# Performance work log

Measured on AMD Instinct MI355X. Metric: run time of the kernel, lower is better.

The kernel has to match this reference:

```python
import jax, jax.numpy as jnp
import numpy as np

B, T, M, DK, DV, S = 64, 256, 64, 128, 256, 128
NSK, NQ = 200, 2000


def _glorot(k, shape):
    lim = np.sqrt(6.0 / (shape[0] + shape[1])).astype(np.float32)
    return jax.random.uniform(k, shape, jnp.float32, -lim, lim)


def setup_inputs() -> dict:
    key = jax.random.key(0)
    ks = jax.random.split(key, 16)
    tn = lambda k, shape: 0.1 * jax.random.truncated_normal(k, -2.0, 2.0, shape, jnp.float32)
    return {
        "q_data": jax.random.randint(ks[0], (B, T), 0, NSK + 1),
        "qa_data": jax.random.randint(ks[1], (B, T), 0, 2 * NSK + 1),
        "s_data": jax.random.randint(ks[2], (B, T), 0, NQ + 1),
        "key_memory": tn(ks[3], (M, DK)),
        "value_memory": tn(ks[4], (M, DV)),
        "Eq": 0.05 * jax.random.normal(ks[5], (NSK + 1, DK), jnp.float32),
        "Eqa": 0.05 * jax.random.normal(ks[6], (2 * NSK + 1, DV), jnp.float32),
        "Es": 0.05 * jax.random.normal(ks[7], (NQ + 1, DK), jnp.float32),
        "We": _glorot(ks[8], (DV, DV)), "be": jnp.zeros((DV,), jnp.float32),
        "Wa": _glorot(ks[9], (DV, DV)), "ba": jnp.zeros((DV,), jnp.float32),
        "Wsa": _glorot(ks[10], (DV, M)), "bsa": jnp.zeros((M,), jnp.float32),
        "Wqd1": _glorot(ks[11], (DK, S)), "bqd1": jnp.zeros((S,), jnp.float32),
        "Wqd": _glorot(ks[12], (S, 1)), "bqd": jnp.zeros((1,), jnp.float32),
        "Wsd1": _glorot(ks[13], (DK, S)), "bsd1": jnp.zeros((S,), jnp.float32),
        "Wsd": _glorot(ks[14], (S, 1)), "bsd": jnp.zeros((1,), jnp.float32),
    }


def reference(q_data, qa_data, s_data, key_memory, value_memory, Eq, Eqa, Es,
              We, be, Wa, ba, Wsa, bsa, Wqd1, bqd1, Wqd, bqd, Wsd1, bsd1, Wsd, bsd):
    b = q_data.shape[0]
    qe = Eq[q_data]    # [B,T,DK]
    qae = Eqa[qa_data]  # [B,T,DV]
    se = Es[s_data]    # [B,T,DK]
    # time-independent precomputation (same math, hoisted out of the loop)
    corr = jax.nn.softmax(jnp.einsum("btk,mk->btm", qe, key_memory), axis=-1)  # [B,T,M]
    erase = qae @ We + be  # [B,T,DV] (activation=None in source)
    add = qae @ Wa + ba    # [B,T,DV]
    qd = jnp.tanh(qe @ Wqd1 + bqd1) @ Wqd + bqd  # [B,T,1]
    sd = jnp.tanh(se @ Wsd1 + bsd1) @ Wsd + bsd  # [B,T,1]

    def step(Mv, x):
        cw, er, ad = x  # [B,M], [B,DV], [B,DV]
        read = jnp.einsum("bm,bmd->bd", cw, Mv)        # read BEFORE write
        sa1 = read @ Wsa + bsa                          # [B,M]
        sa = jnp.sum(cw * sa1, axis=1)                  # [B]
        scale = cw[:, :, None]                          # [B,M,1]
        Mv_new = Mv * (1.0 - er[:, None, :] * scale) + ad[:, None, :] * scale
        return Mv_new, sa

    Mv0 = jnp.broadcast_to(value_memory[None], (b,) + value_memory.shape)
    xs = (corr.transpose(1, 0, 2), erase.transpose(1, 0, 2), add.transpose(1, 0, 2))
    _, sa_t = jax.lax.scan(step, Mv0, xs)  # sa_t: [T,B]
    z = 3.0 * sa_t.T - qd[..., 0] - sd[..., 0]  # [B,T]
    return jax.nn.sigmoid(z)
```

## Files before the change

kernel.cpp:

```cpp
#include <hip/hip_runtime.h>
#include <math.h>

#define B_   64
#define T_   256
#define M_   64
#define DK_  128
#define DV_  256
#define S_   128
#define NQR  201
#define NQAR 401
#define NSR  2001

static __device__ __forceinline__ int imin(int a, int b){ return a < b ? a : b; }

static __device__ __forceinline__ float fast_tanh(float x){
  float e = __expf(2.f * x);
  return 1.f - 2.f / (e + 1.f);
}

template<int CTRL, int RM>
static __device__ __forceinline__ float dppadd(float x) {
  return x + __int_as_float(
      __builtin_amdgcn_update_dpp(0, __float_as_int(x), CTRL, RM, 0xf, true));
}
static __device__ __forceinline__ float wave_sum_lane63(float x) {
  x = dppadd<0x111, 0xf>(x);
  x = dppadd<0x112, 0xf>(x);
  x = dppadd<0x114, 0xf>(x);
  x = dppadd<0x118, 0xf>(x);
  x = dppadd<0x142, 0xa>(x);
  x = dppadd<0x143, 0xc>(x);
  return x;
}

__device__ void corr_role(int blk, const float* __restrict__ Eq,
                          const float* __restrict__ Km,
                          const float* __restrict__ Wsa,
                          const float* __restrict__ bsa,
                          float* __restrict__ corr,
                          float* __restrict__ w2_t,
                          float* __restrict__ csb_t)
{
  __shared__ float eq[4][DK_];
  __shared__ float cwb[4][M_];
  const int w = threadIdx.x >> 6, m = threadIdx.x & 63;
  const int i  = blk * 4 + w;
  const int ic = imin(i, NQR - 1);
  eq[w][m]      = Eq[ic * DK_ + m];
  eq[w][m + 64] = Eq[ic * DK_ + 64 + m];
  float acc = 0.f;
  const float4* kr = (const float4*)(Km + m * DK_);
  #pragma unroll 8
  for (int k4 = 0; k4 < DK_ / 4; ++k4) {
    float4 kv = kr[k4];
    acc = fmaf(eq[w][k4 * 4 + 0], kv.x, acc);
    acc = fmaf(eq[w][k4 * 4 + 1], kv.y, acc);
    acc = fmaf(eq[w][k4 * 4 + 2], kv.z, acc);
    acc = fmaf(eq[w][k4 * 4 + 3], kv.w, acc);
  }
  float mx = acc;
  #pragma unroll
  for (int off = 32; off; off >>= 1) mx = fmaxf(mx, __shfl_xor(mx, off, 64));
  float e = __expf(acc - mx);
  float ssum = e;
  #pragma unroll
  for (int off = 32; off; off >>= 1) ssum += __shfl_xor(ssum, off, 64);
  const float cw = e / ssum;
  if (i < NQR) corr[i * M_ + m] = cw;
  cwb[w][m] = cw;

  float pv = wave_sum_lane63(cw * bsa[m]);
  if (m == 63 && i < NQR) csb_t[i] = pv;

  float aw[4] = {0,0,0,0};
  for (int mm = 0; mm < M_; ++mm) {
    const float c = cwb[w][mm];
    #pragma unroll
    for (int r = 0; r < 4; ++r)
      aw[r] = fmaf(c, Wsa[(r * 64 + m) * M_ + mm], aw[r]);
  }
  if (i < NQR) {
    #pragma unroll
    for (int r = 0; r < 4; ++r) w2_t[i * DV_ + r * 64 + m] = aw[r];
  }
}

__device__ void ea_role(int blk, const float* __restrict__ Eqa,
                        const float* __restrict__ We, const float* __restrict__ be,
                        const float* __restrict__ Wa, const float* __restrict__ ba,
                        float* __restrict__ ert, float* __restrict__ adt)
{
  __shared__ float a[8][DV_];
  const int d  = threadIdx.x;
  const int i0 = blk * 8;
  #pragma unroll
  for (int r = 0; r < 8; ++r) a[r][d] = Eqa[imin(i0 + r, NQAR - 1) * DV_ + d];
  __syncthreads();
  float er[8] = {0,0,0,0,0,0,0,0}, ad[8] = {0,0,0,0,0,0,0,0};
  for (int k = 0; k < DV_; ++k) {
    float we = We[k * DV_ + d];
    float wa = Wa[k * DV_ + d];
    #pragma unroll
    for (int r = 0; r < 8; ++r) {
      er[r] = fmaf(a[r][k], we, er[r]);
      ad[r] = fmaf(a[r][k], wa, ad[r]);
    }
  }
  const float beo = be[d], bao = ba[d];
  #pragma unroll
  for (int r = 0; r < 8; ++r) {
    int i = i0 + r;
    if (i < NQAR) { ert[i * DV_ + d] = er[r] + beo; adt[i * DV_ + d] = ad[r] + bao; }
  }
}

__device__ void mlp_role(int blk, const float* __restrict__ E,
                         const float* __restrict__ W1, const float* __restrict__ b1,
                         const float* __restrict__ W2v, const float* __restrict__ b2,
                         float* __restrict__ outt, int nrows)
{
  __shared__ float e[8 * S_];
  __shared__ float red[8][2];
  const int tid = threadIdx.x;
  const int s = tid & 127, rh = tid >> 7;
  const int i0 = blk * 8;
  #pragma unroll
  for (int j = 0; j < 4; ++j) {
    int x = tid + j * 256;
    int row = imin(i0 + (x >> 7), nrows - 1);
    e[x] = E[row * DK_ + (x & 127)];
  }
  __syncthreads();
  float acc[4] = {0,0,0,0};
  const float* eb = e + rh * 4 * 128;
  for (int k = 0; k < DK_; ++k) {
    float wv = W1[k * S_ + s];
    #pragma unroll
    for (int r = 0; r < 4; ++r) acc[r] = fmaf(eb[r * 128 + k], wv, acc[r]);
  }
  const float b1s = b1[s], w2s = W2v[s];
  float p[4];
  #pragma unroll
  for (int r = 0; r < 4; ++r) p[r] = fast_tanh(acc[r] + b1s) * w2s;
  #pragma unroll
  for (int r = 0; r < 4; ++r) p[r] = wave_sum_lane63(p[r]);
  const int lane = tid & 63;
  const int half = s >> 6;
  if (lane == 63) {
    #pragma unroll
    for (int r = 0; r < 4; ++r) red[rh * 4 + r][half] = p[r];
  }
  __syncthreads();
  if (tid < 8) {
    int i = i0 + tid;
    if (i < nrows) outt[i] = red[tid][0] + red[tid][1] + b2[0];
  }
}

#define NB_CORR 51
#define NB_EA   51
#define NB_QD   26
#define NB_SD   251
#define NB_TOT  (NB_CORR + NB_EA + NB_QD + NB_SD)

__global__ __launch_bounds__(256) void tables_kernel(
    const float* Eq, const float* Km, const float* Wsa, const float* bsa,
    float* corr_t, float* w2_t, float* csb_t,
    const float* Eqa, const float* We, const float* be,
    const float* Wa, const float* ba, float* er_t, float* ad_t,
    const float* Wqd1, const float* bqd1, const float* Wqd, const float* bqd, float* qd_t,
    const float* Es, const float* Wsd1, const float* bsd1, const float* Wsd, const float* bsd, float* sd_t)
{
  int blk = blockIdx.x;
  if (blk < NB_CORR) { corr_role(blk, Eq, Km, Wsa, bsa, corr_t, w2_t, csb_t); return; }
  blk -= NB_CORR;
  if (blk < NB_EA)   { ea_role(blk, Eqa, We, be, Wa, ba, er_t, ad_t); return; }
  blk -= NB_EA;
  if (blk < NB_QD)   { mlp_role(blk, Eq, Wqd1, bqd1, Wqd, bqd, qd_t, NQR); return; }
  blk -= NB_QD;
  mlp_role(blk, Es, Wsd1, bsd1, Wsd, bsd, sd_t, NSR);
}

struct Ops { float4 ca, cb; float er, ad, w2; };

static __device__ __forceinline__ Ops load_ops(
    int q, int qa, int m0, int d,
    const float* __restrict__ corr_t, const float* __restrict__ er_t,
    const float* __restrict__ ad_t, const float* __restrict__ w2_t)
{
  Ops o;
  o.ca = *(const float4*)(corr_t + q * M_ + m0);
  o.cb = *(const float4*)(corr_t + q * M_ + m0 + 4);
  o.er = er_t[qa * DV_ + d];
  o.ad = ad_t[qa * DV_ + d];
  o.w2 = w2_t[q * DV_ + d];
  return o;
}

static __device__ __forceinline__ void scan_step(
    float (&Mv)[8], const Ops& o, float* __restrict__ dst, int dl)
{
  const float cw[8] = {o.ca.x, o.ca.y, o.ca.z, o.ca.w, o.cb.x, o.cb.y, o.cb.z, o.cb.w};
  float r0 = 0.f, r1 = 0.f;
  #pragma unroll
  for (int j = 0; j < 8; ++j) {
    const float c = cw[j];
    if (j & 1) r1 = fmaf(c, Mv[j], r1);
    else       r0 = fmaf(c, Mv[j], r0);
    const float tmp = fmaf(-o.er, Mv[j], o.ad);
    Mv[j] = fmaf(c, tmp, Mv[j]);
  }
  float p = wave_sum_lane63((r0 + r1) * o.w2);
  if (dl == 63) *dst = p;
}

__global__ __launch_bounds__(256) void scan_kernel(
    const int* __restrict__ q_data, const int* __restrict__ qa_data,
    const float* __restrict__ corr_t, const float* __restrict__ er_t,
    const float* __restrict__ ad_t, const float* __restrict__ w2_t,
    const float* __restrict__ Vm, float* __restrict__ sa_part)
{
  const int b  = blockIdx.y;
  const int xx = blockIdx.x;
  const int dq = xx >> 1;
  const int mh = xx & 1;
  const int tid = threadIdx.x;
  const int dl  = tid & 63;
  const int w   = tid >> 6;
  const int mg  = mh * 4 + w;
  const int m0  = __builtin_amdgcn_readfirstlane(mg * 8);
  const int d   = dq * 64 + dl;

  __shared__ int qs[T_];
  __shared__ int qas[T_];
  qs[tid]  = q_data[b * T_ + tid];
  qas[tid] = qa_data[b * T_ + tid];

  float Mv[8];
  #pragma unroll
  for (int j = 0; j < 8; ++j) Mv[j] = Vm[(m0 + j) * DV_ + d];
  __syncthreads();

  float* base = sa_part + (b * T_) * 32 + dq * 8 + mg;

  int q0 = __builtin_amdgcn_readfirstlane(qs[0]);
  int a0 = __builtin_amdgcn_readfirstlane(qas[0]);
  int q1 = __builtin_amdgcn_readfirstlane(qs[1]);
  int a1 = __builtin_amdgcn_readfirstlane(qas[1]);
  Ops o0 = load_ops(q0, a0, m0, d, corr_t, er_t, ad_t, w2_t);
  Ops o1 = load_ops(q1, a1, m0, d, corr_t, er_t, ad_t, w2_t);

  for (int t = 0; t < T_; t += 2) {
    const int t2 = (t + 2) & (T_ - 1), t3 = (t + 3) & (T_ - 1);
    int q2 = __builtin_amdgcn_readfirstlane(qs[t2]);
    int a2 = __builtin_amdgcn_readfirstlane(qas[t2]);
    Ops o2 = load_ops(q2, a2, m0, d, corr_t, er_t, ad_t, w2_t);
    int q3 = __builtin_amdgcn_readfirstlane(qs[t3]);
    int a3 = __builtin_amdgcn_readfirstlane(qas[t3]);
    Ops o3 = load_ops(q3, a3, m0, d, corr_t, er_t, ad_t, w2_t);

    scan_step(Mv, o0, base + t * 32, dl);
    scan_step(Mv, o1, base + (t + 1) * 32, dl);
    o0 = o2; o1 = o3;
  }
}

__global__ __launch_bounds__(256) void final_kernel(
    const int* __restrict__ q_data, const int* __restrict__ s_data,
    const float* __restrict__ sa_part, const float* __restrict__ csb_t,
    const float* __restrict__ qd_t, const float* __restrict__ sd_t,
    float* __restrict__ out)
{
  const int bt = blockIdx.x * 256 + threadIdx.x;
  const float4* sp = (const float4*)(sa_part + bt * 32);
  float s = 0.f;
  #pragma unroll
  for (int j = 0; j < 8; ++j) { float4 v = sp[j]; s += (v.x + v.y) + (v.z + v.w); }
  const int q  = q_data[bt];
  const int si = s_data[bt];
  const float sa = s + csb_t[q];
  const float z = 3.f * sa - qd_t[q] - sd_t[si];
  out[bt] = 1.f / (1.f + __expf(-z));
}

extern "C" void kernel_launch(void* const* d_in, const int* in_sizes, int n_in,
                              void* d_out, int out_size, void* d_ws, size_t ws_size,
                              hipStream_t stream)
{
  const int*   q_data = (const int*)d_in[0];
  const int*   qa_data= (const int*)d_in[1];
  const int*   s_data = (const int*)d_in[2];
  const float* Km     = (const float*)d_in[3];
  const float* Vm     = (const float*)d_in[4];
  const float* Eq     = (const float*)d_in[5];
  const float* Eqa    = (const float*)d_in[6];
  const float* Es     = (const float*)d_in[7];
  const float* We     = (const float*)d_in[8];
  const float* be     = (const float*)d_in[9];
  const float* Wa     = (const float*)d_in[10];
  const float* ba     = (const float*)d_in[11];
  const float* Wsa    = (const float*)d_in[12];
  const float* bsa    = (const float*)d_in[13];
  const float* Wqd1   = (const float*)d_in[14];
  const float* bqd1   = (const float*)d_in[15];
  const float* Wqd    = (const float*)d_in[16];
  const float* bqd    = (const float*)d_in[17];
  const float* Wsd1   = (const float*)d_in[18];
  const float* bsd1   = (const float*)d_in[19];
  const float* Wsd    = (const float*)d_in[20];
  const float* bsd    = (const float*)d_in[21];
  float* out = (float*)d_out;

  float* wsf    = (float*)d_ws;
  float* corr_t = wsf;
  float* w2_t   = corr_t + NQR * M_;
  float* csb_t  = w2_t + NQR * DV_;
  float* er_t   = csb_t + 204;
  float* ad_t   = er_t + NQAR * DV_;
  float* qd_t   = ad_t + NQAR * DV_;
  float* sd_t   = qd_t + 204;
  float* sa_p   = sd_t + 2004;

  tables_kernel<<<NB_TOT, 256, 0, stream>>>(
      Eq, Km, Wsa, bsa, corr_t, w2_t, csb_t,
      Eqa, We, be, Wa, ba, er_t, ad_t,
      Wqd1, bqd1, Wqd, bqd, qd_t,
      Es, Wsd1, bsd1, Wsd, bsd, sd_t);
  scan_kernel<<<dim3(8, B_), 256, 0, stream>>>(q_data, qa_data, corr_t, er_t, ad_t, w2_t, Vm, sa_p);
  final_kernel<<<B_, 256, 0, stream>>>(q_data, s_data, sa_p, csb_t, qd_t, sd_t, out);
}
```

Baseline: 188.5 us.

## Split scan memory rows across twice the waves with deeper index prefetch

Each wave now holds 4 memory rows instead of 8, and scan blocks grow to 512 threads, so the sequential per-step chain per wave is shorter and twice as many waves run in parallel. The token indices come from registers through readlane instead of shared memory with a barrier. Operands are prefetched four steps at a time in two ping-pong batches. Partial sums are written as float4 in a partition-major layout, and the final kernel reduces 64 partials per output instead of 32. The trade-off is twice as many wave reductions and partial-sum writes, plus a larger reduction in the final pass.

```diff
diff --git a/kernel.cpp b/kernel.cpp
--- a/kernel.cpp
+++ b/kernel.cpp
@@ -181,40 +181,46 @@
   mlp_role(blk, Es, Wsd1, bsd1, Wsd, bsd, sd_t, NSR);
 }
 
-struct Ops { float4 ca, cb; float er, ad, w2; };
-
-static __device__ __forceinline__ Ops load_ops(
-    int q, int qa, int m0, int d,
+struct SOps { float4 c; float er, ad, w2; };
+
+static __device__ __forceinline__ void fetch4(
+    int ii, const int4& qq, const int4& qaq, int m0, int d,
     const float* __restrict__ corr_t, const float* __restrict__ er_t,
-    const float* __restrict__ ad_t, const float* __restrict__ w2_t)
-{
-  Ops o;
-  o.ca = *(const float4*)(corr_t + q * M_ + m0);
-  o.cb = *(const float4*)(corr_t + q * M_ + m0 + 4);
-  o.er = er_t[qa * DV_ + d];
-  o.ad = ad_t[qa * DV_ + d];
-  o.w2 = w2_t[q * DV_ + d];
-  return o;
-}
-
-static __device__ __forceinline__ void scan_step(
-    float (&Mv)[8], const Ops& o, float* __restrict__ dst, int dl)
-{
-  const float cw[8] = {o.ca.x, o.ca.y, o.ca.z, o.ca.w, o.cb.x, o.cb.y, o.cb.z, o.cb.w};
-  float r0 = 0.f, r1 = 0.f;
-  #pragma unroll
-  for (int j = 0; j < 8; ++j) {
-    const float c = cw[j];
-    if (j & 1) r1 = fmaf(c, Mv[j], r1);
-    else       r0 = fmaf(c, Mv[j], r0);
-    const float tmp = fmaf(-o.er, Mv[j], o.ad);
-    Mv[j] = fmaf(c, tmp, Mv[j]);
-  }
-  float p = wave_sum_lane63((r0 + r1) * o.w2);
-  if (dl == 63) *dst = p;
-}
-
-__global__ __launch_bounds__(256) void scan_kernel(
+    const float* __restrict__ ad_t, const float* __restrict__ w2_t,
+    SOps (&o)[4])
+{
+  const int q0 = __builtin_amdgcn_readlane(qq.x,  ii);
+  const int q1 = __builtin_amdgcn_readlane(qq.y,  ii);
+  const int q2 = __builtin_amdgcn_readlane(qq.z,  ii);
+  const int q3 = __builtin_amdgcn_readlane(qq.w,  ii);
+  const int a0 = __builtin_amdgcn_readlane(qaq.x, ii);
+  const int a1 = __builtin_amdgcn_readlane(qaq.y, ii);
+  const int a2 = __builtin_amdgcn_readlane(qaq.z, ii);
+  const int a3 = __builtin_amdgcn_readlane(qaq.w, ii);
+  o[0].c = *(const float4*)(corr_t + q0 * M_ + m0);
+  o[1].c = *(const float4*)(corr_t + q1 * M_ + m0);
+  o[2].c = *(const float4*)(corr_t + q2 * M_ + m0);
+  o[3].c = *(const float4*)(corr_t + q3 * M_ + m0);
+  o[0].er = er_t[a0 * DV_ + d];  o[0].ad = ad_t[a0 * DV_ + d];  o[0].w2 = w2_t[q0 * DV_ + d];
+  o[1].er = er_t[a1 * DV_ + d];  o[1].ad = ad_t[a1 * DV_ + d];  o[1].w2 = w2_t[q1 * DV_ + d];
+  o[2].er = er_t[a2 * DV_ + d];  o[2].ad = ad_t[a2 * DV_ + d];  o[2].w2 = w2_t[q2 * DV_ + d];
+  o[3].er = er_t[a3 * DV_ + d];  o[3].ad = ad_t[a3 * DV_ + d];  o[3].w2 = w2_t[q3 * DV_ + d];
+}
+
+static __device__ __forceinline__ float step1(float (&Mv)[4], const SOps& o)
+{
+  float r0 = Mv[0] * o.c.x;
+  float r1 = Mv[1] * o.c.y;
+  r0 = fmaf(Mv[2], o.c.z, r0);
+  r1 = fmaf(Mv[3], o.c.w, r1);
+  Mv[0] = fmaf(o.c.x, fmaf(-o.er, Mv[0], o.ad), Mv[0]);
+  Mv[1] = fmaf(o.c.y, fmaf(-o.er, Mv[1], o.ad), Mv[1]);
+  Mv[2] = fmaf(o.c.z, fmaf(-o.er, Mv[2], o.ad), Mv[2]);
+  Mv[3] = fmaf(o.c.w, fmaf(-o.er, Mv[3], o.ad), Mv[3]);
+  return wave_sum_lane63((r0 + r1) * o.w2);
+}
+
+__global__ __launch_bounds__(512) void scan_kernel(
     const int* __restrict__ q_data, const int* __restrict__ qa_data,
     const float* __restrict__ corr_t, const float* __restrict__ er_t,
     const float* __restrict__ ad_t, const float* __restrict__ w2_t,
@@ -227,41 +233,39 @@
   const int tid = threadIdx.x;
   const int dl  = tid & 63;
   const int w   = tid >> 6;
-  const int mg  = mh * 4 + w;
-  const int m0  = __builtin_amdgcn_readfirstlane(mg * 8);
+  const int mg  = mh * 8 + w;
+  const int m0  = __builtin_amdgcn_readfirstlane(mg * 4);
   const int d   = dq * 64 + dl;
 
-  __shared__ int qs[T_];
-  __shared__ int qas[T_];
-  qs[tid]  = q_data[b * T_ + tid];
-  qas[tid] = qa_data[b * T_ + tid];
-
-  float Mv[8];
-  #pragma unroll
-  for (int j = 0; j < 8; ++j) Mv[j] = Vm[(m0 + j) * DV_ + d];
-  __syncthreads();
-
-  float* base = sa_part + (b * T_) * 32 + dq * 8 + mg;
-
-  int q0 = __builtin_amdgcn_readfirstlane(qs[0]);
-  int a0 = __builtin_amdgcn_readfirstlane(qas[0]);
-  int q1 = __builtin_amdgcn_readfirstlane(qs[1]);
-  int a1 = __builtin_amdgcn_readfirstlane(qas[1]);
-  Ops o0 = load_ops(q0, a0, m0, d, corr_t, er_t, ad_t, w2_t);
-  Ops o1 = load_ops(q1, a1, m0, d, corr_t, er_t, ad_t, w2_t);
-
-  for (int t = 0; t < T_; t += 2) {
-    const int t2 = (t + 2) & (T_ - 1), t3 = (t + 3) & (T_ - 1);
-    int q2 = __builtin_amdgcn_readfirstlane(qs[t2]);
-    int a2 = __builtin_amdgcn_readfirstlane(qas[t2]);
-    Ops o2 = load_ops(q2, a2, m0, d, corr_t, er_t, ad_t, w2_t);
-    int q3 = __builtin_amdgcn_readfirstlane(qs[t3]);
-    int a3 = __builtin_amdgcn_readfirstlane(qas[t3]);
-    Ops o3 = load_ops(q3, a3, m0, d, corr_t, er_t, ad_t, w2_t);
-
-    scan_step(Mv, o0, base + t * 32, dl);
-    scan_step(Mv, o1, base + (t + 1) * 32, dl);
-    o0 = o2; o1 = o3;
+  const int4 qq  = ((const int4*)(q_data  + b * T_))[dl];
+  const int4 qaq = ((const int4*)(qa_data + b * T_))[dl];
+
+  float Mv[4];
+  #pragma unroll
+  for (int j = 0; j < 4; ++j) Mv[j] = Vm[(m0 + j) * DV_ + d];
+
+  float* baseP = sa_part + ((dq * 16 + mg) * B_ + b) * T_;
+
+  SOps A[4], B[4];
+  fetch4(0, qq, qaq, m0, d, corr_t, er_t, ad_t, w2_t, A);
+  fetch4(1, qq, qaq, m0, d, corr_t, er_t, ad_t, w2_t, B);
+
+  for (int i = 0; i < 64; i += 2) {
+    float4 pA;
+    pA.x = step1(Mv, A[0]);
+    pA.y = step1(Mv, A[1]);
+    pA.z = step1(Mv, A[2]);
+    pA.w = step1(Mv, A[3]);
+    fetch4((i + 2) & 63, qq, qaq, m0, d, corr_t, er_t, ad_t, w2_t, A);
+    if (dl == 63) *(float4*)(baseP + 4 * i) = pA;
+
+    float4 pB;
+    pB.x = step1(Mv, B[0]);
+    pB.y = step1(Mv, B[1]);
+    pB.z = step1(Mv, B[2]);
+    pB.w = step1(Mv, B[3]);
+    fetch4((i + 3) & 63, qq, qaq, m0, d, corr_t, er_t, ad_t, w2_t, B);
+    if (dl == 63) *(float4*)(baseP + 4 * i + 4) = pB;
   }
 }
 
@@ -271,11 +275,11 @@
     const float* __restrict__ qd_t, const float* __restrict__ sd_t,
     float* __restrict__ out)
 {
-  const int bt = blockIdx.x * 256 + threadIdx.x;
-  const float4* sp = (const float4*)(sa_part + bt * 32);
+  const int b = blockIdx.x, t = threadIdx.x;
   float s = 0.f;
   #pragma unroll
-  for (int j = 0; j < 8; ++j) { float4 v = sp[j]; s += (v.x + v.y) + (v.z + v.w); }
+  for (int p = 0; p < 64; ++p) s += sa_part[(p * B_ + b) * T_ + t];
+  const int bt = b * T_ + t;
   const int q  = q_data[bt];
   const int si = s_data[bt];
   const float sa = s + csb_t[q];
@@ -326,6 +330,6 @@
       Eqa, We, be, Wa, ba, er_t, ad_t,
       Wqd1, bqd1, Wqd, bqd, qd_t,
       Es, Wsd1, bsd1, Wsd, bsd, sd_t);
-  scan_kernel<<<dim3(8, B_), 256, 0, stream>>>(q_data, qa_data, corr_t, er_t, ad_t, w2_t, Vm, sa_p);
+  scan_kernel<<<dim3(8, B_), 512, 0, stream>>>(q_data, qa_data, corr_t, er_t, ad_t, w2_t, Vm, sa_p);
   final_kernel<<<B_, 256, 0, stream>>>(q_data, s_data, sa_p, csb_t, qd_t, sd_t, out);
 }
```

New measurement: 195.4 us. 3.6% more time.

## Packed-FMA scan with 4-step grouped prefetch and transposed partial-sum layout

Applied to the files above, without the earlier changes.

The scan kernel now keeps memory state as float2 vectors so the update can use packed FMA. It drops the LDS index staging and reads q/qa indices directly as int4 groups of four steps, prefetching two groups of operands ahead. Partial sums are written as float4 every four steps into a [part][B][T] layout, and the final kernel reads that layout with coalesced loads. The corr_role Wsa product also uses float4 loads. The trade-off is higher register pressure, plus a redundant duplicate initialization of Mv, where the first f2 load reads the wrong elements and is then overwritten.

```diff
diff --git a/kernel.cpp b/kernel.cpp
--- a/kernel.cpp
+++ b/kernel.cpp
@@ -10,6 +10,8 @@
 #define NQR  201
 #define NQAR 401
 #define NSR  2001
+
+typedef float f2 __attribute__((ext_vector_type(2)));
 
 static __device__ __forceinline__ int imin(int a, int b){ return a < b ? a : b; }
 
@@ -73,11 +75,15 @@
   if (m == 63 && i < NQR) csb_t[i] = pv;
 
   float aw[4] = {0,0,0,0};
-  for (int mm = 0; mm < M_; ++mm) {
-    const float c = cwb[w][mm];
-    #pragma unroll
-    for (int r = 0; r < 4; ++r)
-      aw[r] = fmaf(c, Wsa[(r * 64 + m) * M_ + mm], aw[r]);
+  for (int mm4 = 0; mm4 < M_ / 4; ++mm4) {
+    #pragma unroll
+    for (int r = 0; r < 4; ++r) {
+      float4 wv = *(const float4*)(Wsa + (r * 64 + m) * M_ + mm4 * 4);
+      aw[r] = fmaf(cwb[w][mm4 * 4 + 0], wv.x, aw[r]);
+      aw[r] = fmaf(cwb[w][mm4 * 4 + 1], wv.y, aw[r]);
+      aw[r] = fmaf(cwb[w][mm4 * 4 + 2], wv.z, aw[r]);
+      aw[r] = fmaf(cwb[w][mm4 * 4 + 3], wv.w, aw[r]);
+    }
   }
   if (i < NQR) {
     #pragma unroll
@@ -181,37 +187,57 @@
   mlp_role(blk, Es, Wsd1, bsd1, Wsd, bsd, sd_t, NSR);
 }
 
-struct Ops { float4 ca, cb; float er, ad, w2; };
-
-static __device__ __forceinline__ Ops load_ops(
+struct IdxG { int4 q, qa; };
+struct OpsS { f2 c01, c23, c45, c67; float er, ad, w2; };
+
+static __device__ __forceinline__ IdxG fetch_idx(
+    int g, const int* __restrict__ q_data, const int* __restrict__ qa_data, int bT)
+{
+  IdxG I;
+  I.q  = *(const int4*)(q_data  + bT + 4 * g);
+  I.qa = *(const int4*)(qa_data + bT + 4 * g);
+  return I;
+}
+
+static __device__ __forceinline__ OpsS fetch_ops1(
     int q, int qa, int m0, int d,
     const float* __restrict__ corr_t, const float* __restrict__ er_t,
     const float* __restrict__ ad_t, const float* __restrict__ w2_t)
 {
-  Ops o;
-  o.ca = *(const float4*)(corr_t + q * M_ + m0);
-  o.cb = *(const float4*)(corr_t + q * M_ + m0 + 4);
+  OpsS o;
+  const f2* cp = (const f2*)(corr_t + q * M_ + m0);
+  o.c01 = cp[0]; o.c23 = cp[1]; o.c45 = cp[2]; o.c67 = cp[3];
   o.er = er_t[qa * DV_ + d];
   o.ad = ad_t[qa * DV_ + d];
   o.w2 = w2_t[q * DV_ + d];
   return o;
 }
 
-static __device__ __forceinline__ void scan_step(
-    float (&Mv)[8], const Ops& o, float* __restrict__ dst, int dl)
-{
-  const float cw[8] = {o.ca.x, o.ca.y, o.ca.z, o.ca.w, o.cb.x, o.cb.y, o.cb.z, o.cb.w};
-  float r0 = 0.f, r1 = 0.f;
-  #pragma unroll
-  for (int j = 0; j < 8; ++j) {
-    const float c = cw[j];
-    if (j & 1) r1 = fmaf(c, Mv[j], r1);
-    else       r0 = fmaf(c, Mv[j], r0);
-    const float tmp = fmaf(-o.er, Mv[j], o.ad);
-    Mv[j] = fmaf(c, tmp, Mv[j]);
-  }
-  float p = wave_sum_lane63((r0 + r1) * o.w2);
-  if (dl == 63) *dst = p;
+static __device__ __forceinline__ void fetch_ops(
+    const IdxG& I, int m0, int d,
+    const float* __restrict__ corr_t, const float* __restrict__ er_t,
+    const float* __restrict__ ad_t, const float* __restrict__ w2_t,
+    OpsS (&o)[4])
+{
+  o[0] = fetch_ops1(I.q.x, I.qa.x, m0, d, corr_t, er_t, ad_t, w2_t);
+  o[1] = fetch_ops1(I.q.y, I.qa.y, m0, d, corr_t, er_t, ad_t, w2_t);
+  o[2] = fetch_ops1(I.q.z, I.qa.z, m0, d, corr_t, er_t, ad_t, w2_t);
+  o[3] = fetch_ops1(I.q.w, I.qa.w, m0, d, corr_t, er_t, ad_t, w2_t);
+}
+
+static __device__ __forceinline__ float stepp(f2 (&Mv)[4], const OpsS& o)
+{
+  const f2 er2 = {o.er, o.er};
+  const f2 ad2 = {o.ad, o.ad};
+  f2 r = o.c01 * Mv[0];
+  Mv[0] = __builtin_elementwise_fma(o.c01, __builtin_elementwise_fma(er2, -Mv[0], ad2), Mv[0]);
+  r = __builtin_elementwise_fma(o.c23, Mv[1], r);
+  Mv[1] = __builtin_elementwise_fma(o.c23, __builtin_elementwise_fma(er2, -Mv[1], ad2), Mv[1]);
+  r = __builtin_elementwise_fma(o.c45, Mv[2], r);
+  Mv[2] = __builtin_elementwise_fma(o.c45, __builtin_elementwise_fma(er2, -Mv[2], ad2), Mv[2]);
+  r = __builtin_elementwise_fma(o.c67, Mv[3], r);
+  Mv[3] = __builtin_elementwise_fma(o.c67, __builtin_elementwise_fma(er2, -Mv[3], ad2), Mv[3]);
+  return wave_sum_lane63((r.x + r.y) * o.w2);
 }
 
 __global__ __launch_bounds__(256) void scan_kernel(
@@ -220,48 +246,56 @@
     const float* __restrict__ ad_t, const float* __restrict__ w2_t,
     const float* __restrict__ Vm, float* __restrict__ sa_part)
 {
-  const int b  = blockIdx.y;
-  const int xx = blockIdx.x;
-  const int dq = xx >> 1;
-  const int mh = xx & 1;
+  const int b   = blockIdx.y;
+  const int dq  = blockIdx.x >> 1;
+  const int mh  = blockIdx.x & 1;
   const int tid = threadIdx.x;
   const int dl  = tid & 63;
   const int w   = tid >> 6;
   const int mg  = mh * 4 + w;
   const int m0  = __builtin_amdgcn_readfirstlane(mg * 8);
   const int d   = dq * 64 + dl;
-
-  __shared__ int qs[T_];
-  __shared__ int qas[T_];
-  qs[tid]  = q_data[b * T_ + tid];
-  qas[tid] = qa_data[b * T_ + tid];
-
-  float Mv[8];
-  #pragma unroll
-  for (int j = 0; j < 8; ++j) Mv[j] = Vm[(m0 + j) * DV_ + d];
-  __syncthreads();
-
-  float* base = sa_part + (b * T_) * 32 + dq * 8 + mg;
-
-  int q0 = __builtin_amdgcn_readfirstlane(qs[0]);
-  int a0 = __builtin_amdgcn_readfirstlane(qas[0]);
-  int q1 = __builtin_amdgcn_readfirstlane(qs[1]);
-  int a1 = __builtin_amdgcn_readfirstlane(qas[1]);
-  Ops o0 = load_ops(q0, a0, m0, d, corr_t, er_t, ad_t, w2_t);
-  Ops o1 = load_ops(q1, a1, m0, d, corr_t, er_t, ad_t, w2_t);
-
-  for (int t = 0; t < T_; t += 2) {
-    const int t2 = (t + 2) & (T_ - 1), t3 = (t + 3) & (T_ - 1);
-    int q2 = __builtin_amdgcn_readfirstlane(qs[t2]);
-    int a2 = __builtin_amdgcn_readfirstlane(qas[t2]);
-    Ops o2 = load_ops(q2, a2, m0, d, corr_t, er_t, ad_t, w2_t);
-    int q3 = __builtin_amdgcn_readfirstlane(qs[t3]);
-    int a3 = __builtin_amdgcn_readfirstlane(qas[t3]);
-    Ops o3 = load_ops(q3, a3, m0, d, corr_t, er_t, ad_t, w2_t);
-
-    scan_step(Mv, o0, base + t * 32, dl);
-    scan_step(Mv, o1, base + (t + 1) * 32, dl);
-    o0 = o2; o1 = o3;
+  const int bT  = b * T_;
+
+  f2 Mv[4];
+  #pragma unroll
+  for (int j = 0; j < 4; ++j)
+    Mv[j] = *(const f2*)(Vm + (m0 + 2 * j) * DV_ + d) ;
+
+  #pragma unroll
+  for (int j = 0; j < 4; ++j) {
+    Mv[j].x = Vm[(m0 + 2 * j) * DV_ + d];
+    Mv[j].y = Vm[(m0 + 2 * j + 1) * DV_ + d];
+  }
+
+  float* baseP = sa_part + ((dq * 8 + mg) * B_ + b) * T_;
+
+  IdxG i0 = fetch_idx(0, q_data, qa_data, bT);
+  IdxG i1 = fetch_idx(1, q_data, qa_data, bT);
+  OpsS A[4], Bo[4];
+  fetch_ops(i0, m0, d, corr_t, er_t, ad_t, w2_t, A);
+  fetch_ops(i1, m0, d, corr_t, er_t, ad_t, w2_t, Bo);
+  i0 = fetch_idx(2, q_data, qa_data, bT);
+  i1 = fetch_idx(3, q_data, qa_data, bT);
+
+  for (int g = 0; g < 64; g += 2) {
+    float4 pA;
+    pA.x = stepp(Mv, A[0]);
+    pA.y = stepp(Mv, A[1]);
+    pA.z = stepp(Mv, A[2]);
+    pA.w = stepp(Mv, A[3]);
+    fetch_ops(i0, m0, d, corr_t, er_t, ad_t, w2_t, A);
+    i0 = fetch_idx((g + 4) & 63, q_data, qa_data, bT);
+    if (dl == 63) *(float4*)(baseP + 4 * g) = pA;
+
+    float4 pB;
+    pB.x = stepp(Mv, Bo[0]);
+    pB.y = stepp(Mv, Bo[1]);
+    pB.z = stepp(Mv, Bo[2]);
+    pB.w = stepp(Mv, Bo[3]);
+    fetch_ops(i1, m0, d, corr_t, er_t, ad_t, w2_t, Bo);
+    i1 = fetch_idx((g + 5) & 63, q_data, qa_data, bT);
+    if (dl == 63) *(float4*)(baseP + 4 * g + 4) = pB;
   }
 }
 
@@ -271,11 +305,11 @@
     const float* __restrict__ qd_t, const float* __restrict__ sd_t,
     float* __restrict__ out)
 {
-  const int bt = blockIdx.x * 256 + threadIdx.x;
-  const float4* sp = (const float4*)(sa_part + bt * 32);
+  const int b = blockIdx.x, t = threadIdx.x;
   float s = 0.f;
   #pragma unroll
-  for (int j = 0; j < 8; ++j) { float4 v = sp[j]; s += (v.x + v.y) + (v.z + v.w); }
+  for (int p = 0; p < 32; ++p) s += sa_part[(p * B_ + b) * T_ + t];
+  const int bt = b * T_ + t;
   const int q  = q_data[bt];
   const int si = s_data[bt];
   const float sa = s + csb_t[q];
```

New measurement: 221.8 us. +17.7%, slower.
